# Kernel tuning notes

Measured on AMD Instinct MI355X. Metric: run time of the kernel, lower is better.

The kernel has to match this reference:

```python
import jax, jax.numpy as jnp
import numpy as np

B, F, H = 512, 64, 256
INPUT_LEN, TARGET_LEN = 128, 128


def _gru_step(h, xt, Wih, Whh, bih, bhh):
    # PyTorch GRU cell: gates ordered [r, z, n]
    gi = xt @ Wih.T + bih            # [B, 3H]
    gh = h @ Whh.T + bhh             # [B, 3H]
    ir, iz, inn = jnp.split(gi, 3, axis=-1)
    hr, hz, hn = jnp.split(gh, 3, axis=-1)
    r = jax.nn.sigmoid(ir + hr)
    z = jax.nn.sigmoid(iz + hz)
    n = jnp.tanh(inn + r * hn)
    return (1.0 - z) * n + z * h


def setup_inputs() -> dict:
    key = jax.random.key(0)
    ks = jax.random.split(key, 12)
    s_in = 1.0 / np.sqrt(H)
    x = jax.random.normal(ks[0], (B, INPUT_LEN + TARGET_LEN, F), dtype=jnp.float32)
    u = lambda k, shp: jax.random.uniform(k, shp, jnp.float32, -s_in, s_in)
    return {
        "x": x,
        "enc_Wih": u(ks[1], (3 * H, F)), "enc_Whh": u(ks[2], (3 * H, H)),
        "enc_bih": u(ks[3], (3 * H,)), "enc_bhh": u(ks[4], (3 * H,)),
        "dec_Wih": u(ks[5], (3 * H, F)), "dec_Whh": u(ks[6], (3 * H, H)),
        "dec_bih": u(ks[7], (3 * H,)), "dec_bhh": u(ks[8], (3 * H,)),
        "reg_W": u(ks[9], (F, H)), "reg_b": u(ks[10], (F,)),
        "input_len": INPUT_LEN, "target_len": TARGET_LEN,
    }


def reference(x, enc_Wih, enc_Whh, enc_bih, enc_bhh,
              dec_Wih, dec_Whh, dec_bih, dec_bhh,
              reg_W, reg_b, input_len, target_len):
    source_seq = x[:, :input_len, :]                       # [B, Tin, F]
    b = source_seq.shape[0]

    # Encoder GRU over source sequence, h0 = 0
    def enc_step(h, xt):
        h = _gru_step(h, xt, enc_Wih, enc_Whh, enc_bih, enc_bhh)
        return h, None
    h0 = jnp.zeros((b, enc_Whh.shape[1]), dtype=x.dtype)
    h_enc, _ = jax.lax.scan(enc_step, h0, source_seq.transpose(1, 0, 2))

    # Decoder: eval mode -> teacher forcing prob 0, always feed back own output
    dec_in0 = source_seq[:, -1, :]                         # [B, F]
    def dec_step(carry, _):
        h, inp = carry
        h = _gru_step(h, inp, dec_Wih, dec_Whh, dec_bih, dec_bhh)
        out = h @ reg_W.T + reg_b                          # [B, F]
        return (h, out), out
    (_, _), outs = jax.lax.scan(dec_step, (h_enc, dec_in0), None, length=target_len)
    return outs.transpose(1, 0, 2)                         # [B, Tout, F]
```

## Files before the change

kernel.cpp:

```cpp
#include <hip/hip_runtime.h>
#include <math.h>

#define Bsz 512
#define Fsz 64
#define Hsz 256
#define TSTEPS 128
#define G3 768

#define BG 16
#define HB 16
#define NBLK 256
#define NTHR 256

#define RED_SLOTS 40
#define OFF_B (RED_SLOTS*64*16)
#define SMEM_BYTES (OFF_B + 512)

typedef float f32x4 __attribute__((ext_vector_type(4)));
typedef short s16x8 __attribute__((ext_vector_type(8)));
typedef unsigned int  u32x4 __attribute__((ext_vector_type(4)));

#define MF(a,b,c) __builtin_amdgcn_mfma_f32_16x16x32_bf16(a,b,c,0,0,0)

static __device__ __forceinline__ unsigned short bf16_rne(float f){
    union { float f; unsigned u; } v; v.f = f;
    return (unsigned short)((v.u + 0x7FFFu + ((v.u >> 16) & 1u)) >> 16);
}
static __device__ __forceinline__ float bf16_to_f(unsigned short h){
    union { unsigned u; float f; } v; v.u = ((unsigned)h) << 16; return v.f;
}
static __device__ __forceinline__ void split8(const float* p, s16x8& hi, s16x8& lo){
    #pragma unroll
    for (int t = 0; t < 8; ++t){
        float f = p[t];
        unsigned short h = bf16_rne(f);
        hi[t] = (short)h;
        lo[t] = (short)bf16_rne(f - bf16_to_f(h));
    }
}
static __device__ __forceinline__ float sigmoidf_(float v){ return 1.0f/(1.0f + expf(-v)); }

__device__ __forceinline__ u32x4 load_sys_b128u(const unsigned* p){
    u32x4 r;
    asm volatile("global_load_dwordx4 %0, %1, off sc0 sc1" : "=v"(r) : "v"(p) : "memory");
    return r;
}
__device__ __forceinline__ unsigned load_sys_b32u_nw(const unsigned* p){
    unsigned r;
    asm volatile("global_load_dword %0, %1, off sc0 sc1" : "=v"(r) : "v"(p) : "memory");
    return r;
}
__device__ __forceinline__ void store_sys_b32u(unsigned* p, unsigned v){
    asm volatile("global_store_dword %0, %1, off sc0 sc1" :: "v"(p), "v"(v) : "memory");
}
__device__ __forceinline__ int load_sys_i32(const int* p){
    int r;
    asm volatile("global_load_dword %0, %1, off sc0 sc1\n\ts_waitcnt vmcnt(0)"
                 : "=v"(r) : "v"(p) : "memory");
    return r;
}
__device__ __forceinline__ void waitcnt0(){ asm volatile("s_waitcnt vmcnt(0)" ::: "memory"); }
__device__ __forceinline__ void regbar(u32x4& v){ asm volatile("" : "+v"(v)); }
__device__ __forceinline__ void regbar32(unsigned& v){ asm volatile("" : "+v"(v)); }

static __device__ __forceinline__ void unpack8(const u32x4 a, const u32x4 b, s16x8& hi, s16x8& lo){
    #pragma unroll
    for (int e = 0; e < 4; ++e){
        hi[e]   = (short)(a[e] >> 16);  lo[e]   = (short)(a[e] & 0xFFFFu);
        hi[4+e] = (short)(b[e] >> 16);  lo[4+e] = (short)(b[e] & 0xFFFFu);
    }
}

extern "C" __global__ void gru_setup(const float* __restrict__ x,
                                     const float* __restrict__ dWih,
                                     const float* __restrict__ dbih,
                                     const float* __restrict__ regW,
                                     const float* __restrict__ regb,
                                     float* __restrict__ Mw,
                                     float* __restrict__ cfold,
                                     float* __restrict__ gi0)
{
    int idx = blockIdx.x*blockDim.x + threadIdx.x;
    if (idx < G3*Hsz) {
        int g = idx >> 8, j = idx & 255;
        float a = 0.f;
        #pragma unroll 8
        for (int f = 0; f < Fsz; ++f) a += dWih[g*Fsz + f]*regW[f*Hsz + j];
        Mw[idx] = a;
    } else if (idx < G3*Hsz + G3) {
        int g = idx - G3*Hsz;
        float a = dbih[g];
        #pragma unroll 8
        for (int f = 0; f < Fsz; ++f) a += dWih[g*Fsz + f]*regb[f];
        cfold[g] = a;
    } else {
        int e = idx - (G3*Hsz + G3);
        if (e < Bsz*G3) {
            int b = e / G3, g = e - b*G3;
            const float* xp = x + (size_t)b*(256*64) + 127*64;
            float a = dbih[g];
            #pragma unroll 8
            for (int f = 0; f < Fsz; ++f) a += xp[f]*dWih[g*Fsz + f];
            gi0[e] = a;
        }
    }
}

extern "C" __global__ void __launch_bounds__(NTHR, 1)
gru_persistent(const float* __restrict__ x,
               const float* __restrict__ eWih, const float* __restrict__ eWhh,
               const float* __restrict__ ebih, const float* __restrict__ ebhh,
               const float* __restrict__ dWhh, const float* __restrict__ dbhh,
               const float* __restrict__ Mw,   const float* __restrict__ cfold,
               const float* __restrict__ gi0,  const float* __restrict__ regW,
               const float* __restrict__ regb,
               unsigned* __restrict__ hbuf, unsigned* __restrict__ canary,
               float* __restrict__ out)
{
    extern __shared__ char lds[];
    f32x4* s_redv = (f32x4*)lds;
    float* s_bias = (float*)(lds + OFF_B);
    float* s_dbh  = s_bias + 64;
    float* s_b3   = s_bias + 112;

    const int tid  = threadIdx.x;
    const int wv   = tid >> 6;
    const int lane = tid & 63;
    const int quad = lane >> 4;
    const int lcol = lane & 15;
    const int bg   = blockIdx.x & 15;
    const int hb   = blockIdx.x >> 4;
    const int hcol = hb*16 + lcol;
    const int mw   = wv & 1;
    const int kh   = wv >> 1;
    const int jb   = kh*2;
    const int hr0  = mw*16 + quad*4 + jb;
    const f32x4 z4 = {0.f, 0.f, 0.f, 0.f};

    unsigned* mycan = canary + ((size_t)bg*64 + hb*4 + wv)*4;
    const int* canp = (const int*)canary + ((size_t)bg*64 + lane)*4;
    const int  can_mine = ((lane >> 2) == hb);

    s16x8 wfh[3][2], wfl[3][2];
    s16x8 ufh[3], ufl[3];
    s16x8 rwh[2], rwl[2];
    #pragma unroll
    for (int g = 0; g < 3; ++g){
        #pragma unroll
        for (int q = 0; q < 2; ++q)
            split8(eWhh + (size_t)(g*256 + hcol)*256 + wv*64 + q*32 + quad*8,
                   wfh[g][q], wfl[g][q]);
        split8(eWih + (size_t)(g*256 + hcol)*64 + kh*32 + quad*8, ufh[g], ufl[g]);
    }
    if (tid < 16){
        int c = hb*16 + tid;
        s_bias[tid]    = ebih[c]       + ebhh[c];
        s_bias[16+tid] = ebih[256+c]   + ebhh[256+c];
        s_bias[32+tid] = ebih[512+c];
        s_bias[48+tid] = ebhh[512+c];
    }
    __syncthreads();

    for (int g = 0; g <= 2*TSTEPS; ++g){
        const bool enc  = (g < TSTEPS);
        const bool last = (g == 2*TSTEPS);
        const unsigned* hin = hbuf + (size_t)(g & 1)*Bsz*Hsz;
        unsigned* hout = hbuf + (size_t)((g+1) & 1)*Bsz*Hsz;

        if (g == TSTEPS){
            #pragma unroll
            for (int gg = 0; gg < 3; ++gg)
                #pragma unroll
                for (int q = 0; q < 2; ++q)
                    split8(dWhh + (size_t)(gg*256 + hcol)*256 + wv*64 + q*32 + quad*8,
                           wfh[gg][q], wfl[gg][q]);
            #pragma unroll
            for (int q = 0; q < 2; ++q){
                split8(Mw   + (size_t)(2*256 + hcol)*256 + wv*64 + q*32 + quad*8,
                       ufh[q], ufl[q]);
                split8(regW + (size_t)(hb*4 + (lcol & 3))*256 + wv*64 + q*32 + quad*8,
                       rwh[q], rwl[q]);
            }
            if (tid < 16){
                int c = hb*16 + tid;
                s_bias[tid]    = cfold[c]     + dbhh[c];
                s_bias[16+tid] = cfold[256+c] + dbhh[256+c];
                s_bias[32+tid] = cfold[512+c];
                s_dbh[tid]     = dbhh[c];
                s_dbh[16+tid]  = dbhh[256+c];
                s_dbh[32+tid]  = dbhh[512+c];
            }
            if (tid < 4) s_b3[tid] = regb[hb*4 + tid];
            __syncthreads();
        }
        if (g == TSTEPS + 1){
            #pragma unroll
            for (int gg = 0; gg < 2; ++gg)
                #pragma unroll
                for (int q = 0; q < 2; ++q){
                    float tmp[8];
                    const float* pa = dWhh + (size_t)(gg*256 + hcol)*256 + wv*64 + q*32 + quad*8;
                    const float* pb = Mw   + (size_t)(gg*256 + hcol)*256 + wv*64 + q*32 + quad*8;
                    #pragma unroll
                    for (int t2 = 0; t2 < 8; ++t2) tmp[t2] = pa[t2] + pb[t2];
                    split8(tmp, wfh[gg][q], wfl[gg][q]);
                }
        }

        f32x4 aR[2], aZ[2], aNi[2], aNh[2], oa[2];
        oa[0] = z4; oa[1] = z4;
        if (wv == 0 && !last){
            if (g == TSTEPS){
                #pragma unroll
                for (int m = 0; m < 2; ++m)
                    #pragma unroll
                    for (int j = 0; j < 4; ++j){
                        int grow_ = bg*32 + m*16 + quad*4 + j;
                        const float* gp = gi0 + (size_t)grow_*G3 + hcol;
                        aR[m][j]  = gp[0]   + s_dbh[lcol];
                        aZ[m][j]  = gp[256] + s_dbh[16+lcol];
                        aNi[m][j] = gp[512];
                        aNh[m][j] = s_dbh[32+lcol];
                    }
            } else {
                float bR = s_bias[lcol], bZ = s_bias[16+lcol], bNi = s_bias[32+lcol];
                float bNh = enc ? s_bias[48+lcol] : s_dbh[32+lcol];
                #pragma unroll
                for (int m = 0; m < 2; ++m){
                    aR[m] = (f32x4){bR,bR,bR,bR}; aZ[m] = (f32x4){bZ,bZ,bZ,bZ};
                    aNi[m] = (f32x4){bNi,bNi,bNi,bNi}; aNh[m] = (f32x4){bNh,bNh,bNh,bNh};
                }
            }
        } else {
            #pragma unroll
            for (int m = 0; m < 2; ++m){ aR[m]=z4; aZ[m]=z4; aNi[m]=z4; aNh[m]=z4; }
        }

        f32x4 xv0, xv1;
        if (enc){
            const float* xp = x + (size_t)(bg*32 + mw*16 + lcol)*(256*64)
                                + (size_t)g*64 + kh*32 + quad*8;
            xv0 = *(const f32x4*)xp;
            xv1 = *(const f32x4*)(xp + 4);
        }

        if (g){
            while (1){
                int v = load_sys_i32(canp);
                if (__all(can_mine | (v >= g))) break;
                __builtin_amdgcn_s_sleep(1);
            }
        }

        const unsigned* ab = hin + (size_t)(bg*32 + lcol)*256 + wv*64 + quad*8;
        u32x4 t[8];
        #pragma unroll
        for (int m = 0; m < 2; ++m)
            #pragma unroll
            for (int q = 0; q < 2; ++q)
                #pragma unroll
                for (int h4 = 0; h4 < 2; ++h4)
                    t[m*4+q*2+h4] = load_sys_b128u(ab + m*4096 + q*32 + h4*4);
        const unsigned* hoA = hin + (size_t)(bg*32 + hr0)*256 + hcol;
        unsigned ho0 = load_sys_b32u_nw(hoA);
        unsigned ho1 = load_sys_b32u_nw(hoA + 256);

        if (enc){
            float xf[8];
            #pragma unroll
            for (int e = 0; e < 4; ++e){ xf[e] = xv0[e]; xf[4+e] = xv1[e]; }
            s16x8 xh, xl;
            split8(xf, xh, xl);
            #define XMF(M) { \
                aR[M] =MF(xh,ufh[0],aR[M]);  aR[M] =MF(xh,ufl[0],aR[M]);  aR[M] =MF(xl,ufh[0],aR[M]);  \
                aZ[M] =MF(xh,ufh[1],aZ[M]);  aZ[M] =MF(xh,ufl[1],aZ[M]);  aZ[M] =MF(xl,ufh[1],aZ[M]);  \
                aNi[M]=MF(xh,ufh[2],aNi[M]); aNi[M]=MF(xh,ufl[2],aNi[M]); aNi[M]=MF(xl,ufh[2],aNi[M]); }
            if (mw == 0) XMF(0) else XMF(1)
            #undef XMF
        }

        waitcnt0();
        #pragma unroll
        for (int jj = 0; jj < 8; ++jj) regbar(t[jj]);
        regbar32(ho0); regbar32(ho1);

        #pragma unroll
        for (int m = 0; m < 2; ++m){
            #pragma unroll
            for (int q = 0; q < 2; ++q){
                s16x8 ah, al;
                unpack8(t[m*4+q*2], t[m*4+q*2+1], ah, al);
                if (!last){
                    aR[m]=MF(ah,wfh[0][q],aR[m]); aR[m]=MF(ah,wfl[0][q],aR[m]); aR[m]=MF(al,wfh[0][q],aR[m]);
                    aZ[m]=MF(ah,wfh[1][q],aZ[m]); aZ[m]=MF(ah,wfl[1][q],aZ[m]); aZ[m]=MF(al,wfh[1][q],aZ[m]);
                    aNh[m]=MF(ah,wfh[2][q],aNh[m]); aNh[m]=MF(ah,wfl[2][q],aNh[m]); aNh[m]=MF(al,wfh[2][q],aNh[m]);
                    if (!enc && g > TSTEPS){
                        aNi[m]=MF(ah,ufh[q],aNi[m]); aNi[m]=MF(ah,ufl[q],aNi[m]); aNi[m]=MF(al,ufh[q],aNi[m]);
                    }
                }
                if (g >= TSTEPS + 1){
                    oa[m]=MF(ah,rwh[q],oa[m]); oa[m]=MF(ah,rwl[q],oa[m]); oa[m]=MF(al,rwh[q],oa[m]);
                }
            }
        }

        if (!last){
            f32x4* rp = s_redv + (size_t)(wv*8)*64 + lane;
            rp[0]   = aR[0]; rp[64]  = aZ[0]; rp[128] = aNi[0]; rp[192] = aNh[0];
            rp[256] = aR[1]; rp[320] = aZ[1]; rp[384] = aNi[1]; rp[448] = aNh[1];
        }
        if (g >= TSTEPS + 1){
            f32x4* op = s_redv + (size_t)(32 + wv*2)*64 + lane;
            op[0] = oa[0]; op[64] = oa[1];
        }
        __syncthreads();

        if (!last){
            f32x4 R = z4, Z = z4, Ni = z4, Nh = z4;
            #pragma unroll
            for (int w2 = 0; w2 < 4; ++w2){
                const f32x4* rp = s_redv + (size_t)(w2*8 + mw*4)*64 + lane;
                R += rp[0]; Z += rp[64]; Ni += rp[128]; Nh += rp[192];
            }
            #define EW(J, HW, RO) { \
                float r = sigmoidf_(R[J]); \
                float z = sigmoidf_(Z[J]); \
                float n = tanhf(Ni[J] + r*Nh[J]); \
                float hold = bf16_to_f((unsigned short)((HW) >> 16)) \
                           + bf16_to_f((unsigned short)((HW) & 0xFFFFu)); \
                float hv = (1.0f - z)*n + z*hold; \
                unsigned short p1 = bf16_rne(hv); \
                unsigned short p0 = bf16_rne(hv - bf16_to_f(p1)); \
                store_sys_b32u(hout + (size_t)(bg*32 + hr0 + RO)*256 + hcol, \
                               (((unsigned)p1) << 16) | (unsigned)p0); }
            if (jb == 0){ EW(0, ho0, 0); EW(1, ho1, 1); }
            else        { EW(2, ho0, 0); EW(3, ho1, 1); }
            #undef EW
        }

        if (g >= TSTEPS + 1 && wv >= 2){
            const int m2 = wv - 2;
            float b3 = s_b3[lcol & 3];
            f32x4 ot = {b3, b3, b3, b3};
            #pragma unroll
            for (int w2 = 0; w2 < 4; ++w2)
                ot += s_redv[(size_t)(32 + w2*2 + m2)*64 + lane];
            if (lcol < 4){
                const int oidx = g - TSTEPS - 1;
                #pragma unroll
                for (int j = 0; j < 4; ++j)
                    out[(size_t)(bg*32 + m2*16 + quad*4 + j)*(TSTEPS*Fsz)
                        + (size_t)oidx*Fsz + hb*4 + lcol] = ot[j];
            }
        }

        if (!last){
            waitcnt0();
            if (lane == 0) store_sys_b32u(mycan, (unsigned)(g + 1));
        }
        __syncthreads();
    }
}

extern "C" void kernel_launch(void* const* d_in, const int* in_sizes, int n_in,
                              void* d_out, int out_size, void* d_ws, size_t ws_size,
                              hipStream_t stream)
{
    (void)in_sizes; (void)n_in; (void)out_size; (void)ws_size;
    const float* x    = (const float*)d_in[0];
    const float* eWih = (const float*)d_in[1];
    const float* eWhh = (const float*)d_in[2];
    const float* ebih = (const float*)d_in[3];
    const float* ebhh = (const float*)d_in[4];
    const float* dWih = (const float*)d_in[5];
    const float* dWhh = (const float*)d_in[6];
    const float* dbih = (const float*)d_in[7];
    const float* dbhh = (const float*)d_in[8];
    const float* regW = (const float*)d_in[9];
    const float* regb = (const float*)d_in[10];
    float* out = (float*)d_out;

    unsigned* hbuf = (unsigned*)d_ws;
    float* Mw    = (float*)d_ws + 2*Bsz*Hsz;
    float* gi0   = Mw + G3*Hsz;
    float* cfold = gi0 + Bsz*G3;
    unsigned* canary = (unsigned*)(cfold + 1024);

    hipMemsetAsync(hbuf, 0, (size_t)Bsz*Hsz*sizeof(unsigned), stream);
    hipMemsetAsync(canary, 0, (size_t)BG*64*4*sizeof(unsigned), stream);

    hipLaunchKernelGGL(gru_setup, dim3(2307), dim3(256), 0, stream,
                       x, dWih, dbih, regW, regb, Mw, cfold, gi0);

    hipFuncSetAttribute((const void*)gru_persistent,
                        hipFuncAttributeMaxDynamicSharedMemorySize, SMEM_BYTES);

    void* args[] = { (void*)&x, (void*)&eWih, (void*)&eWhh, (void*)&ebih, (void*)&ebhh,
                     (void*)&dWhh, (void*)&dbhh, (void*)&Mw, (void*)&cfold, (void*)&gi0,
                     (void*)&regW, (void*)&regb, (void*)&hbuf, (void*)&canary, (void*)&out };
    hipError_t rc = hipLaunchCooperativeKernel((const void*)gru_persistent,
                                               dim3(NBLK), dim3(NTHR), args,
                                               SMEM_BYTES, stream);
    if (rc != hipSuccess) {
        hipLaunchKernelGGL(gru_persistent, dim3(NBLK), dim3(NTHR), SMEM_BYTES, stream,
                           x, eWih, eWhh, ebih, ebhh, dWhh, dbhh, Mw, cfold, gi0,
                           regW, regb, hbuf, canary, out);
    }
}
```

Before: 1.162 ms.

## Tag hidden-state words for in-band readiness and halve block count with wider blocks

Restructures the persistent GRU kernel to use 128 blocks of 512 threads, each owning 32 hidden columns, with input weights moved to LDS. Each h word's low mantissa bits now carry a 2-bit step tag, so consumers can check readiness directly from the loaded data and fall back to canary polling only when stale. The previous h value is kept in registers instead of reloaded. LDS reduction buffers are double-buffered to drop the trailing barrier. Fast exp2/rcp-based sigmoid and tanh are also added. This trades slight precision loss in the low bf16 part and more complex synchronization for fewer global round trips per step.

Result: slower. 1.419 ms (+22.1%).

```diff
diff --git a/kernel.cpp b/kernel.cpp
--- a/kernel.cpp
+++ b/kernel.cpp
@@ -8,13 +8,14 @@
 #define G3 768
 
 #define BG 16
-#define HB 16
-#define NBLK 256
-#define NTHR 256
-
-#define RED_SLOTS 40
-#define OFF_B (RED_SLOTS*64*16)
-#define SMEM_BYTES (OFF_B + 512)
+#define HB 8
+#define NBLK 128
+#define NTHR 512
+
+#define OFF_AUX   131072
+#define OFF_OUT   (OFF_AUX + 16*1024)
+#define OFF_B     (OFF_AUX + 24*1024)
+#define SMEM_BYTES (OFF_B + 1024)
 
 typedef float f32x4 __attribute__((ext_vector_type(4)));
 typedef short s16x8 __attribute__((ext_vector_type(8)));
@@ -38,16 +39,16 @@
         lo[t] = (short)bf16_rne(f - bf16_to_f(h));
     }
 }
-static __device__ __forceinline__ float sigmoidf_(float v){ return 1.0f/(1.0f + expf(-v)); }
+static __device__ __forceinline__ float sigmoidf_(float v){
+    return __builtin_amdgcn_rcpf(1.0f + __builtin_amdgcn_exp2f(-1.44269504f*v));
+}
+static __device__ __forceinline__ float tanhf_(float v){
+    return 1.0f - 2.0f*__builtin_amdgcn_rcpf(1.0f + __builtin_amdgcn_exp2f(2.88539008f*v));
+}
 
 __device__ __forceinline__ u32x4 load_sys_b128u(const unsigned* p){
     u32x4 r;
     asm volatile("global_load_dwordx4 %0, %1, off sc0 sc1" : "=v"(r) : "v"(p) : "memory");
-    return r;
-}
-__device__ __forceinline__ unsigned load_sys_b32u_nw(const unsigned* p){
-    unsigned r;
-    asm volatile("global_load_dword %0, %1, off sc0 sc1" : "=v"(r) : "v"(p) : "memory");
     return r;
 }
 __device__ __forceinline__ void store_sys_b32u(unsigned* p, unsigned v){
@@ -61,7 +62,6 @@
 }
 __device__ __forceinline__ void waitcnt0(){ asm volatile("s_waitcnt vmcnt(0)" ::: "memory"); }
 __device__ __forceinline__ void regbar(u32x4& v){ asm volatile("" : "+v"(v)); }
-__device__ __forceinline__ void regbar32(unsigned& v){ asm volatile("" : "+v"(v)); }
 
 static __device__ __forceinline__ void unpack8(const u32x4 a, const u32x4 b, s16x8& hi, s16x8& lo){
     #pragma unroll
@@ -118,247 +118,269 @@
                float* __restrict__ out)
 {
     extern __shared__ char lds[];
-    f32x4* s_redv = (f32x4*)lds;
+    f32x4* s_red  = (f32x4*)lds;
+    s16x8* s_aux  = (s16x8*)(lds + OFF_AUX);
+    f32x4* s_outv = (f32x4*)(lds + OFF_OUT);
     float* s_bias = (float*)(lds + OFF_B);
-    float* s_dbh  = s_bias + 64;
-    float* s_b3   = s_bias + 112;
 
     const int tid  = threadIdx.x;
     const int wv   = tid >> 6;
     const int lane = tid & 63;
     const int quad = lane >> 4;
     const int lcol = lane & 15;
+    const int m    = wv & 1;
+    const int kq   = wv >> 1;
     const int bg   = blockIdx.x & 15;
     const int hb   = blockIdx.x >> 4;
-    const int hcol = hb*16 + lcol;
-    const int mw   = wv & 1;
-    const int kh   = wv >> 1;
-    const int jb   = kh*2;
-    const int hr0  = mw*16 + quad*4 + jb;
-    const f32x4 z4 = {0.f, 0.f, 0.f, 0.f};
-
-    unsigned* mycan = canary + ((size_t)bg*64 + hb*4 + wv)*4;
-    const int* canp = (const int*)canary + ((size_t)bg*64 + lane)*4;
-    const int  can_mine = ((lane >> 2) == hb);
-
-    s16x8 wfh[3][2], wfl[3][2];
-    s16x8 ufh[3], ufl[3];
-    s16x8 rwh[2], rwl[2];
+    const int m_o  = hb >> 2, nc = hb & 3;
+    const int n2e  = kq >> 1;
+    const int jb2  = (kq & 1)*2;
+    const int r0   = m*16 + quad*4 + jb2;
+    const int colL = n2e*16 + lcol;
+    const int ce   = hb*32 + colL;
+    const f32x4 z4 = {0.f,0.f,0.f,0.f};
+
+    unsigned* mycan = canary + bg*64 + hb*8 + wv;
+    const int* fp = (const int*)canary + bg*64 + (kq*2 + ((lane>>3)&1))*8 + (lane & 7);
+
+    s16x8 wfh[3][2][2], wfl[3][2][2];
     #pragma unroll
-    for (int g = 0; g < 3; ++g){
+    for (int gg = 0; gg < 3; ++gg)
         #pragma unroll
-        for (int q = 0; q < 2; ++q)
-            split8(eWhh + (size_t)(g*256 + hcol)*256 + wv*64 + q*32 + quad*8,
-                   wfh[g][q], wfl[g][q]);
-        split8(eWih + (size_t)(g*256 + hcol)*64 + kh*32 + quad*8, ufh[g], ufl[g]);
-    }
-    if (tid < 16){
-        int c = hb*16 + tid;
-        s_bias[tid]    = ebih[c]       + ebhh[c];
-        s_bias[16+tid] = ebih[256+c]   + ebhh[256+c];
-        s_bias[32+tid] = ebih[512+c];
-        s_bias[48+tid] = ebhh[512+c];
+        for (int n2 = 0; n2 < 2; ++n2)
+            #pragma unroll
+            for (int kt = 0; kt < 2; ++kt)
+                split8(eWhh + (size_t)(gg*256 + hb*32 + n2*16 + lcol)*256 + kq*64 + kt*32 + quad*8,
+                       wfh[gg][n2][kt], wfl[gg][n2][kt]);
+    s16x8 mfh[2][2], mfl[2][2];
+
+    for (int u = wv; u < 12; u += 8){
+        int gg = u >> 2, n2 = (u >> 1) & 1, kx = u & 1;
+        s16x8 hi, lo;
+        split8(eWih + (size_t)(gg*256 + hb*32 + n2*16 + lcol)*64 + kx*32 + quad*8, hi, lo);
+        s_aux[u*64 + lane] = hi;
+        s_aux[(12+u)*64 + lane] = lo;
+    }
+    if (tid < 32){
+        int c = hb*32 + tid;
+        s_bias[tid]     = ebih[c]     + ebhh[c];
+        s_bias[32+tid]  = ebih[256+c] + ebhh[256+c];
+        s_bias[64+tid]  = ebih[512+c];
+        s_bias[96+tid]  = ebhh[512+c];
     }
     __syncthreads();
+
+    float hold0 = 0.f, hold1 = 0.f;
 
     for (int g = 0; g <= 2*TSTEPS; ++g){
         const bool enc  = (g < TSTEPS);
         const bool last = (g == 2*TSTEPS);
+        const int  p    = g & 1;
+        const unsigned tag  = (unsigned)((g >> 1) & 3);
+        const unsigned otag = (unsigned)(((g+1) >> 1) & 3);
         const unsigned* hin = hbuf + (size_t)(g & 1)*Bsz*Hsz;
         unsigned* hout = hbuf + (size_t)((g+1) & 1)*Bsz*Hsz;
 
+        float gr0=0.f, gz0=0.f, gn0=0.f, gr1=0.f, gz1=0.f, gn1=0.f;
+
         if (g == TSTEPS){
+            __syncthreads();
             #pragma unroll
             for (int gg = 0; gg < 3; ++gg)
                 #pragma unroll
-                for (int q = 0; q < 2; ++q)
-                    split8(dWhh + (size_t)(gg*256 + hcol)*256 + wv*64 + q*32 + quad*8,
-                           wfh[gg][q], wfl[gg][q]);
-            #pragma unroll
-            for (int q = 0; q < 2; ++q){
-                split8(Mw   + (size_t)(2*256 + hcol)*256 + wv*64 + q*32 + quad*8,
-                       ufh[q], ufl[q]);
-                split8(regW + (size_t)(hb*4 + (lcol & 3))*256 + wv*64 + q*32 + quad*8,
-                       rwh[q], rwl[q]);
-            }
-            if (tid < 16){
-                int c = hb*16 + tid;
-                s_bias[tid]    = cfold[c]     + dbhh[c];
-                s_bias[16+tid] = cfold[256+c] + dbhh[256+c];
-                s_bias[32+tid] = cfold[512+c];
-                s_dbh[tid]     = dbhh[c];
-                s_dbh[16+tid]  = dbhh[256+c];
-                s_dbh[32+tid]  = dbhh[512+c];
-            }
-            if (tid < 4) s_b3[tid] = regb[hb*4 + tid];
+                for (int n2 = 0; n2 < 2; ++n2)
+                    #pragma unroll
+                    for (int kt = 0; kt < 2; ++kt)
+                        split8(dWhh + (size_t)(gg*256 + hb*32 + n2*16 + lcol)*256 + kq*64 + kt*32 + quad*8,
+                               wfh[gg][n2][kt], wfl[gg][n2][kt]);
+            #pragma unroll
+            for (int n2 = 0; n2 < 2; ++n2)
+                #pragma unroll
+                for (int kt = 0; kt < 2; ++kt)
+                    split8(Mw + (size_t)(512 + hb*32 + n2*16 + lcol)*256 + kq*64 + kt*32 + quad*8,
+                           mfh[n2][kt], mfl[n2][kt]);
+            {
+                s16x8 hi, lo;
+                split8(regW + (size_t)(nc*16 + lcol)*256 + (wv>>1)*64 + (wv&1)*32 + quad*8, hi, lo);
+                s_aux[wv*64 + lane] = hi;
+                s_aux[(8+wv)*64 + lane] = lo;
+            }
+            if (tid < 32){
+                int c = hb*32 + tid;
+                s_bias[tid]     = cfold[c]     + dbhh[c];
+                s_bias[32+tid]  = cfold[256+c] + dbhh[256+c];
+                s_bias[64+tid]  = cfold[512+c];
+                s_bias[96+tid]  = dbhh[512+c];
+                s_bias[128+tid] = dbhh[c];
+                s_bias[160+tid] = dbhh[256+c];
+            }
+            if (tid < 16) s_bias[192+tid] = regb[nc*16 + tid];
             __syncthreads();
+            const float* gp0 = gi0 + (size_t)(bg*32 + r0)*G3 + hb*32 + colL;
+            gr0 = gp0[0]; gz0 = gp0[256]; gn0 = gp0[512];
+            gr1 = gp0[G3]; gz1 = gp0[G3+256]; gn1 = gp0[G3+512];
         }
         if (g == TSTEPS + 1){
             #pragma unroll
             for (int gg = 0; gg < 2; ++gg)
                 #pragma unroll
-                for (int q = 0; q < 2; ++q){
-                    float tmp[8];
-                    const float* pa = dWhh + (size_t)(gg*256 + hcol)*256 + wv*64 + q*32 + quad*8;
-                    const float* pb = Mw   + (size_t)(gg*256 + hcol)*256 + wv*64 + q*32 + quad*8;
+                for (int n2 = 0; n2 < 2; ++n2)
                     #pragma unroll
-                    for (int t2 = 0; t2 < 8; ++t2) tmp[t2] = pa[t2] + pb[t2];
-                    split8(tmp, wfh[gg][q], wfl[gg][q]);
-                }
-        }
-
-        f32x4 aR[2], aZ[2], aNi[2], aNh[2], oa[2];
-        oa[0] = z4; oa[1] = z4;
-        if (wv == 0 && !last){
-            if (g == TSTEPS){
-                #pragma unroll
-                for (int m = 0; m < 2; ++m)
-                    #pragma unroll
-                    for (int j = 0; j < 4; ++j){
-                        int grow_ = bg*32 + m*16 + quad*4 + j;
-                        const float* gp = gi0 + (size_t)grow_*G3 + hcol;
-                        aR[m][j]  = gp[0]   + s_dbh[lcol];
-                        aZ[m][j]  = gp[256] + s_dbh[16+lcol];
-                        aNi[m][j] = gp[512];
-                        aNh[m][j] = s_dbh[32+lcol];
+                    for (int kt = 0; kt < 2; ++kt){
+                        float tmp[8];
+                        size_t o = (size_t)(gg*256 + hb*32 + n2*16 + lcol)*256 + kq*64 + kt*32 + quad*8;
+                        #pragma unroll
+                        for (int t2 = 0; t2 < 8; ++t2) tmp[t2] = dWhh[o+t2] + Mw[o+t2];
+                        split8(tmp, wfh[gg][n2][kt], wfl[gg][n2][kt]);
                     }
-            } else {
-                float bR = s_bias[lcol], bZ = s_bias[16+lcol], bNi = s_bias[32+lcol];
-                float bNh = enc ? s_bias[48+lcol] : s_dbh[32+lcol];
-                #pragma unroll
-                for (int m = 0; m < 2; ++m){
-                    aR[m] = (f32x4){bR,bR,bR,bR}; aZ[m] = (f32x4){bZ,bZ,bZ,bZ};
-                    aNi[m] = (f32x4){bNi,bNi,bNi,bNi}; aNh[m] = (f32x4){bNh,bNh,bNh,bNh};
-                }
-            }
-        } else {
-            #pragma unroll
-            for (int m = 0; m < 2; ++m){ aR[m]=z4; aZ[m]=z4; aNi[m]=z4; aNh[m]=z4; }
-        }
-
-        f32x4 xv0, xv1;
-        if (enc){
-            const float* xp = x + (size_t)(bg*32 + mw*16 + lcol)*(256*64)
-                                + (size_t)g*64 + kh*32 + quad*8;
-            xv0 = *(const f32x4*)xp;
-            xv1 = *(const f32x4*)(xp + 4);
-        }
-
-        if (g){
-            while (1){
-                int v = load_sys_i32(canp);
-                if (__all(can_mine | (v >= g))) break;
-                __builtin_amdgcn_s_sleep(1);
-            }
-        }
-
-        const unsigned* ab = hin + (size_t)(bg*32 + lcol)*256 + wv*64 + quad*8;
-        u32x4 t[8];
-        #pragma unroll
-        for (int m = 0; m < 2; ++m)
-            #pragma unroll
-            for (int q = 0; q < 2; ++q)
-                #pragma unroll
-                for (int h4 = 0; h4 < 2; ++h4)
-                    t[m*4+q*2+h4] = load_sys_b128u(ab + m*4096 + q*32 + h4*4);
-        const unsigned* hoA = hin + (size_t)(bg*32 + hr0)*256 + hcol;
-        unsigned ho0 = load_sys_b32u_nw(hoA);
-        unsigned ho1 = load_sys_b32u_nw(hoA + 256);
-
-        if (enc){
+        }
+
+        f32x4 aR[2], aZ[2], aNi[2], aNh[2], oa;
+        aR[0]=z4; aR[1]=z4; aZ[0]=z4; aZ[1]=z4;
+        aNi[0]=z4; aNi[1]=z4; aNh[0]=z4; aNh[1]=z4; oa=z4;
+
+        const unsigned* ab = hin + (size_t)(bg*32 + m*16 + lcol)*256 + kq*64 + quad*8;
+        u32x4 t[4];
+        t[0] = load_sys_b128u(ab);
+        t[1] = load_sys_b128u(ab + 4);
+        t[2] = load_sys_b128u(ab + 32);
+        t[3] = load_sys_b128u(ab + 36);
+
+        if (enc && kq < 2){
+            const float* xp = x + (size_t)(bg*32 + m*16 + lcol)*(256*64) + (size_t)g*64 + kq*32 + quad*8;
+            f32x4 xv0 = *(const f32x4*)xp, xv1 = *(const f32x4*)(xp + 4);
             float xf[8];
             #pragma unroll
             for (int e = 0; e < 4; ++e){ xf[e] = xv0[e]; xf[4+e] = xv1[e]; }
             s16x8 xh, xl;
             split8(xf, xh, xl);
-            #define XMF(M) { \
-                aR[M] =MF(xh,ufh[0],aR[M]);  aR[M] =MF(xh,ufl[0],aR[M]);  aR[M] =MF(xl,ufh[0],aR[M]);  \
-                aZ[M] =MF(xh,ufh[1],aZ[M]);  aZ[M] =MF(xh,ufl[1],aZ[M]);  aZ[M] =MF(xl,ufh[1],aZ[M]);  \
-                aNi[M]=MF(xh,ufh[2],aNi[M]); aNi[M]=MF(xh,ufl[2],aNi[M]); aNi[M]=MF(xl,ufh[2],aNi[M]); }
-            if (mw == 0) XMF(0) else XMF(1)
-            #undef XMF
-        }
-
-        waitcnt0();
+            #pragma unroll
+            for (int n2 = 0; n2 < 2; ++n2){
+                s16x8 bh, bl;
+                bh = s_aux[(n2*2+kq)*64 + lane];      bl = s_aux[(12+n2*2+kq)*64 + lane];
+                aR[n2]=MF(xh,bh,aR[n2]); aR[n2]=MF(xh,bl,aR[n2]); aR[n2]=MF(xl,bh,aR[n2]);
+                bh = s_aux[(4+n2*2+kq)*64 + lane];    bl = s_aux[(16+n2*2+kq)*64 + lane];
+                aZ[n2]=MF(xh,bh,aZ[n2]); aZ[n2]=MF(xh,bl,aZ[n2]); aZ[n2]=MF(xl,bh,aZ[n2]);
+                bh = s_aux[(8+n2*2+kq)*64 + lane];    bl = s_aux[(20+n2*2+kq)*64 + lane];
+                aNi[n2]=MF(xh,bh,aNi[n2]); aNi[n2]=MF(xh,bl,aNi[n2]); aNi[n2]=MF(xl,bh,aNi[n2]);
+            }
+        }
+
+        #define UPD() { \
+            _Pragma("unroll") \
+            for (int i = 0; i < 4; ++i) \
+                if (!((done >> i) & 1u)){ \
+                    unsigned xx = (t[i][0]^tag)|(t[i][1]^tag)|(t[i][2]^tag)|(t[i][3]^tag); \
+                    if ((xx & 3u) == 0u) done |= (1u << i); } }
+        {
+            unsigned done = 0;
+            waitcnt0();
+            #pragma unroll
+            for (int i = 0; i < 4; ++i) regbar(t[i]);
+            UPD();
+            if (!__all((int)(done == 0xFu))){
+                int v = (int)g;
+                while (1){
+                    if (lane < 16) v = load_sys_i32(fp);
+                    if (__all((int)((lane >= 16) | (v >= (int)g)))) break;
+                    __builtin_amdgcn_s_sleep(1);
+                }
+                while (1){
+                    if (!((done >> 0) & 1u)) t[0] = load_sys_b128u(ab);
+                    if (!((done >> 1) & 1u)) t[1] = load_sys_b128u(ab + 4);
+                    if (!((done >> 2) & 1u)) t[2] = load_sys_b128u(ab + 32);
+                    if (!((done >> 3) & 1u)) t[3] = load_sys_b128u(ab + 36);
+                    waitcnt0();
+                    #pragma unroll
+                    for (int i = 0; i < 4; ++i) regbar(t[i]);
+                    UPD();
+                    if (__all((int)(done == 0xFu))) break;
+                    __builtin_amdgcn_s_sleep(1);
+                }
+            }
+        }
+        #undef UPD
+
         #pragma unroll
-        for (int jj = 0; jj < 8; ++jj) regbar(t[jj]);
-        regbar32(ho0); regbar32(ho1);
-
-        #pragma unroll
-        for (int m = 0; m < 2; ++m){
-            #pragma unroll
-            for (int q = 0; q < 2; ++q){
-                s16x8 ah, al;
-                unpack8(t[m*4+q*2], t[m*4+q*2+1], ah, al);
-                if (!last){
-                    aR[m]=MF(ah,wfh[0][q],aR[m]); aR[m]=MF(ah,wfl[0][q],aR[m]); aR[m]=MF(al,wfh[0][q],aR[m]);
-                    aZ[m]=MF(ah,wfh[1][q],aZ[m]); aZ[m]=MF(ah,wfl[1][q],aZ[m]); aZ[m]=MF(al,wfh[1][q],aZ[m]);
-                    aNh[m]=MF(ah,wfh[2][q],aNh[m]); aNh[m]=MF(ah,wfl[2][q],aNh[m]); aNh[m]=MF(al,wfh[2][q],aNh[m]);
+        for (int kt = 0; kt < 2; ++kt){
+            s16x8 ah, al;
+            unpack8(t[kt*2], t[kt*2+1], ah, al);
+            if (!last){
+                #pragma unroll
+                for (int n2 = 0; n2 < 2; ++n2){
+                    aR[n2]=MF(ah,wfh[0][n2][kt],aR[n2]); aR[n2]=MF(ah,wfl[0][n2][kt],aR[n2]); aR[n2]=MF(al,wfh[0][n2][kt],aR[n2]);
+                    aZ[n2]=MF(ah,wfh[1][n2][kt],aZ[n2]); aZ[n2]=MF(ah,wfl[1][n2][kt],aZ[n2]); aZ[n2]=MF(al,wfh[1][n2][kt],aZ[n2]);
+                    aNh[n2]=MF(ah,wfh[2][n2][kt],aNh[n2]); aNh[n2]=MF(ah,wfl[2][n2][kt],aNh[n2]); aNh[n2]=MF(al,wfh[2][n2][kt],aNh[n2]);
                     if (!enc && g > TSTEPS){
-                        aNi[m]=MF(ah,ufh[q],aNi[m]); aNi[m]=MF(ah,ufl[q],aNi[m]); aNi[m]=MF(al,ufh[q],aNi[m]);
+                        aNi[n2]=MF(ah,mfh[n2][kt],aNi[n2]); aNi[n2]=MF(ah,mfl[n2][kt],aNi[n2]); aNi[n2]=MF(al,mfh[n2][kt],aNi[n2]);
                     }
                 }
-                if (g >= TSTEPS + 1){
-                    oa[m]=MF(ah,rwh[q],oa[m]); oa[m]=MF(ah,rwl[q],oa[m]); oa[m]=MF(al,rwh[q],oa[m]);
-                }
+            }
+            if (g >= TSTEPS + 1 && m == m_o){
+                s16x8 bh = s_aux[(kq*2+kt)*64 + lane];
+                s16x8 bl = s_aux[(8+kq*2+kt)*64 + lane];
+                oa = MF(ah,bh,oa); oa = MF(ah,bl,oa); oa = MF(al,bh,oa);
             }
         }
 
         if (!last){
-            f32x4* rp = s_redv + (size_t)(wv*8)*64 + lane;
-            rp[0]   = aR[0]; rp[64]  = aZ[0]; rp[128] = aNi[0]; rp[192] = aNh[0];
-            rp[256] = aR[1]; rp[320] = aZ[1]; rp[384] = aNi[1]; rp[448] = aNh[1];
-        }
-        if (g >= TSTEPS + 1){
-            f32x4* op = s_redv + (size_t)(32 + wv*2)*64 + lane;
-            op[0] = oa[0]; op[64] = oa[1];
-        }
+            f32x4* bp = s_red + (size_t)((p*8 + wv)*8)*64 + lane;
+            bp[0]   = aR[0];  bp[64]  = aR[1];
+            bp[128] = aZ[0];  bp[192] = aZ[1];
+            bp[256] = aNi[0]; bp[320] = aNi[1];
+            bp[384] = aNh[0]; bp[448] = aNh[1];
+        }
+        if (g >= TSTEPS + 1 && m == m_o)
+            s_outv[(size_t)(p*4 + kq)*64 + lane] = oa;
         __syncthreads();
 
         if (!last){
             f32x4 R = z4, Z = z4, Ni = z4, Nh = z4;
             #pragma unroll
-            for (int w2 = 0; w2 < 4; ++w2){
-                const f32x4* rp = s_redv + (size_t)(w2*8 + mw*4)*64 + lane;
-                R += rp[0]; Z += rp[64]; Ni += rp[128]; Nh += rp[192];
-            }
-            #define EW(J, HW, RO) { \
-                float r = sigmoidf_(R[J]); \
-                float z = sigmoidf_(Z[J]); \
-                float n = tanhf(Ni[J] + r*Nh[J]); \
-                float hold = bf16_to_f((unsigned short)((HW) >> 16)) \
-                           + bf16_to_f((unsigned short)((HW) & 0xFFFFu)); \
-                float hv = (1.0f - z)*n + z*hold; \
+            for (int k2 = 0; k2 < 4; ++k2){
+                const f32x4* bp = s_red + (size_t)((p*8 + (k2*2+m))*8)*64 + lane;
+                R  += bp[(0+n2e)*64];
+                Z  += bp[(2+n2e)*64];
+                Ni += bp[(4+n2e)*64];
+                Nh += bp[(6+n2e)*64];
+            }
+            const float bNh_ = s_bias[96+colL];
+            #define EW(JJ, GR, GZ, GN, HOLD) { \
+                const int j = jb2 + JJ; \
+                float r, z, n; \
+                if (g == TSTEPS){ \
+                    r = sigmoidf_(R[j] + GR + s_bias[128+colL]); \
+                    z = sigmoidf_(Z[j] + GZ + s_bias[160+colL]); \
+                    n = tanhf_(GN + r*(Nh[j] + bNh_)); \
+                } else { \
+                    r = sigmoidf_(R[j] + s_bias[colL]); \
+                    z = sigmoidf_(Z[j] + s_bias[32+colL]); \
+                    n = tanhf_(Ni[j] + s_bias[64+colL] + r*(Nh[j] + bNh_)); \
+                } \
+                float hv = (1.0f - z)*n + z*HOLD; \
                 unsigned short p1 = bf16_rne(hv); \
-                unsigned short p0 = bf16_rne(hv - bf16_to_f(p1)); \
-                store_sys_b32u(hout + (size_t)(bg*32 + hr0 + RO)*256 + hcol, \
-                               (((unsigned)p1) << 16) | (unsigned)p0); }
-            if (jb == 0){ EW(0, ho0, 0); EW(1, ho1, 1); }
-            else        { EW(2, ho0, 0); EW(3, ho1, 1); }
+                unsigned short p0 = (unsigned short)((bf16_rne(hv - bf16_to_f(p1)) & 0xFFFCu) | otag); \
+                store_sys_b32u(hout + (size_t)(bg*32 + r0 + JJ)*256 + ce, \
+                               (((unsigned)p1) << 16) | (unsigned)p0); \
+                HOLD = bf16_to_f(p1) + bf16_to_f(p0); }
+            EW(0, gr0, gz0, gn0, hold0);
+            EW(1, gr1, gz1, gn1, hold1);
             #undef EW
-        }
-
-        if (g >= TSTEPS + 1 && wv >= 2){
-            const int m2 = wv - 2;
-            float b3 = s_b3[lcol & 3];
-            f32x4 ot = {b3, b3, b3, b3};
-            #pragma unroll
-            for (int w2 = 0; w2 < 4; ++w2)
-                ot += s_redv[(size_t)(32 + w2*2 + m2)*64 + lane];
-            if (lcol < 4){
-                const int oidx = g - TSTEPS - 1;
-                #pragma unroll
-                for (int j = 0; j < 4; ++j)
-                    out[(size_t)(bg*32 + m2*16 + quad*4 + j)*(TSTEPS*Fsz)
-                        + (size_t)oidx*Fsz + hb*4 + lcol] = ot[j];
-            }
-        }
-
-        if (!last){
-            waitcnt0();
             if (lane == 0) store_sys_b32u(mycan, (unsigned)(g + 1));
         }
-        __syncthreads();
+
+        if (g >= TSTEPS + 1 && wv == m_o){
+            float rb = s_bias[192 + lcol];
+            f32x4 ot = {rb, rb, rb, rb};
+            #pragma unroll
+            for (int k2 = 0; k2 < 4; ++k2)
+                ot += s_outv[(size_t)(p*4 + k2)*64 + lane];
+            const int oi = g - TSTEPS - 1;
+            #pragma unroll
+            for (int j = 0; j < 4; ++j)
+                out[(size_t)(bg*32 + m_o*16 + quad*4 + j)*(TSTEPS*Fsz)
+                    + (size_t)oi*Fsz + nc*16 + lcol] = ot[j];
+        }
     }
 }
 
@@ -383,11 +405,12 @@
     unsigned* hbuf = (unsigned*)d_ws;
     float* Mw    = (float*)d_ws + 2*Bsz*Hsz;
     float* gi0   = Mw + G3*Hsz;
-    float* cfold = gi0 + Bsz*G3;
+    float* cfold = gi0 + (size_t)Bsz*G3;
     unsigned* canary = (unsigned*)(cfold + 1024);
 
     hipMemsetAsync(hbuf, 0, (size_t)Bsz*Hsz*sizeof(unsigned), stream);
-    hipMemsetAsync(canary, 0, (size_t)BG*64*4*sizeof(unsigned), stream);
+    hipMemsetAsync(hbuf + (size_t)Bsz*Hsz, 3, (size_t)Bsz*Hsz*sizeof(unsigned), stream);
+    hipMemsetAsync(canary, 0, (size_t)BG*64*sizeof(unsigned), stream);
 
     hipLaunchKernelGGL(gru_setup, dim3(2307), dim3(256), 0, stream,
                        x, dWih, dbih, regW, regb, Mw, cfold, gi0);
```
